# Kernel tuning notes

Hardware: AMD Instinct MI355X
Metric: run time of the kernel (lower is better)

## Reference

```python
import jax, jax.numpy as jnp
import numpy as np
import math

B, N, D_IN, D_OUT, H = 8, 1024, 512, 512, 8
DH = D_OUT // H  # 64
SCALE = math.sqrt(DH)

def setup_inputs() -> dict:
    key = jax.random.key(0)
    ks = jax.random.split(key, 10)
    s_in = 1.0 / math.sqrt(D_IN)
    s_out = 1.0 / math.sqrt(D_OUT)
    return {
        "x": jax.random.normal(ks[0], (B, N, D_IN), dtype=jnp.float32),
        "Wq": jax.random.uniform(ks[1], (D_IN, D_OUT), jnp.float32, -s_in, s_in),
        "bq": jnp.zeros((D_OUT,), jnp.float32),
        "Wk": jax.random.uniform(ks[2], (D_IN, D_OUT), jnp.float32, -s_in, s_in),
        "bk": jnp.zeros((D_OUT,), jnp.float32),
        "Wv": jax.random.uniform(ks[3], (D_IN, D_OUT), jnp.float32, -s_in, s_in),
        "bv": jnp.zeros((D_OUT,), jnp.float32),
        "Wo": jax.random.uniform(ks[4], (D_OUT, D_OUT), jnp.float32, -s_out, s_out),
        "bo": jnp.zeros((D_OUT,), jnp.float32),
        # external distance-based positional bias buffer (num_heads, N, N)
        "pos_bias": 0.01 * jax.random.normal(ks[5], (H, N, N), dtype=jnp.float32),
    }

def reference(x, Wq, bq, Wk, bk, Wv, bv, Wo, bo, pos_bias):
    Bx, Nx, _ = x.shape
    # QKV projections -> (B, H, N, DH)
    def split_heads(t):
        return t.reshape(Bx, Nx, H, DH).transpose(0, 2, 1, 3)
    q = split_heads(x @ Wq + bq)
    k = split_heads(x @ Wk + bk)
    v = split_heads(x @ Wv + bv)
    # scaled dot-product scores with additive positional bias
    scores = jnp.einsum('bhnd,bhmd->bhnm', q, k) / SCALE + pos_bias[None]
    attn = jax.nn.softmax(scores, axis=-1)  # dropout p=0 (eval)
    out = jnp.einsum('bhnm,bhmd->bhnd', attn, v)
    out = out.transpose(0, 2, 1, 3).reshape(Bx, Nx, D_OUT)  # concat heads
    return out @ Wo + bo
```

## Files before the change

### kernel.cpp

```cpp
#include <hip/hip_runtime.h>
#include <hip/hip_bf16.h>
#include <stdint.h>


typedef __attribute__((ext_vector_type(4))) float f32x4;
typedef __attribute__((ext_vector_type(8))) short s16x8;
typedef __attribute__((ext_vector_type(4))) unsigned short u16x4;
typedef __attribute__((ext_vector_type(8))) unsigned short u16x8;

union FragAB { s16x8 v; u16x4 h[2]; unsigned u[4]; };

#define LOG2E 1.44269504089f
#define QSCALE (0.125f * LOG2E)

__device__ __forceinline__ unsigned short f2b(float f) {
  unsigned u = __builtin_bit_cast(unsigned, f);
  u = (u + 0x7FFFu + ((u >> 16) & 1u)) >> 16;
  return (unsigned short)u;
}
__device__ __forceinline__ unsigned cvt_pk(float a, float b) {
  unsigned r;
  asm("v_cvt_pk_bf16_f32 %0, %1, %2" : "=v"(r) : "v"(a), "v"(b));
  return r;
}
__device__ __forceinline__ void gl_lds16(const unsigned short* g, unsigned short* l) {
  __builtin_amdgcn_global_load_lds(
      (const __attribute__((address_space(1))) unsigned int*)(g),
      (__attribute__((address_space(3))) unsigned int*)(l), 16, 0, 0);
}

__global__ __launch_bounds__(256) void prep_k(const float* __restrict__ x,
                                              unsigned short* __restrict__ xb,
                                              const float* __restrict__ W0,
                                              const float* __restrict__ W1,
                                              const float* __restrict__ W2,
                                              const float* __restrict__ W3,
                                              unsigned short* __restrict__ Wt) {
  __shared__ float ld[64][68];
  const int t = threadIdx.x;
  if (blockIdx.x < 4096) {
    int idx = blockIdx.x * 256 + t;
    f32x4 v = ((const f32x4*)x)[idx];
    u16x4 o;
#pragma unroll
    for (int j = 0; j < 4; j++) o[j] = f2b(v[j]);
    ((u16x4*)xb)[idx] = o;
    return;
  }
  const int bid2 = blockIdx.x - 4096;
  const int widx = bid2 >> 6;
  const int tile = bid2 & 63;
  const int trow = tile >> 3, tcol = tile & 7;
  const float* W = widx == 0 ? W0 : widx == 1 ? W1 : widx == 2 ? W2 : W3;
  const int r = t >> 2, cc = (t & 3) * 16;
  const float* src = W + (size_t)(trow * 64 + r) * 512 + tcol * 64 + cc;
#pragma unroll
  for (int u = 0; u < 4; u++)
    ((f32x4*)&ld[r][cc])[u] = ((const f32x4*)src)[u];
  __syncthreads();
  unsigned short* dst = Wt + ((size_t)widx << 18) + (size_t)(tcol * 64 + r) * 512 +
                        trow * 64 + cc;
#pragma unroll
  for (int u = 0; u < 4; u++) {
    u16x4 o;
#pragma unroll
    for (int e = 0; e < 4; e++) o[e] = f2b(ld[cc + u * 4 + e][r]);
    ((u16x4*)dst)[u] = o;
  }
}

__global__ __launch_bounds__(256, 2) void gemm_qkv_k(const unsigned short* __restrict__ A,
                                                     const unsigned short* __restrict__ Bt,
                                                     const float* __restrict__ bq,
                                                     const float* __restrict__ bk,
                                                     const float* __restrict__ bv,
                                                     unsigned short* __restrict__ outp) {
  __shared__ unsigned short SM[2][2][128][32];
  const int tid = threadIdx.x;
  const int lane = tid & 63;
  const int w = tid >> 6;
  const int wm = w >> 1, wn = w & 1;
  const int g = lane >> 4, c = lane & 15;
  const int bn0 = (blockIdx.x % 12) * 128;
  const int bm0 = (blockIdx.x / 12) * 128;

  f32x4 acc[4][4];
#pragma unroll
  for (int i = 0; i < 4; i++)
#pragma unroll
    for (int j = 0; j < 4; j++) acc[i][j] = f32x4{0.f, 0.f, 0.f, 0.f};

  auto stage = [&](int buf, int kt) {
#pragma unroll
    for (int j = 0; j < 2; j++) {
      const int qb = (j * 4 + w) * 64;
      const int chunk = qb + lane;
      const int row = chunk >> 2, slot = chunk & 3;
      gl_lds16(A + (size_t)(bm0 + row) * 512 + kt * 32 + slot * 8,
               &SM[buf][0][0][0] + qb * 8);
      gl_lds16(Bt + (size_t)(bn0 + row) * 512 + kt * 32 + slot * 8,
               &SM[buf][1][0][0] + qb * 8);
    }
  };

  stage(0, 0);
  asm volatile("s_waitcnt vmcnt(0)" ::: "memory");
  __syncthreads();

  for (int kt = 0; kt < 16; ++kt) {
    const int cb = kt & 1;
    if (kt < 15) stage(cb ^ 1, kt + 1);

    FragAB af[4], bf[4];
#pragma unroll
    for (int mi = 0; mi < 4; mi++) {
      const u16x4* p = (const u16x4*)&SM[cb][0][wm * 64 + mi * 16 + c][g * 8];
      af[mi].h[0] = p[0]; af[mi].h[1] = p[1];
    }
#pragma unroll
    for (int ni = 0; ni < 4; ni++) {
      const u16x4* p = (const u16x4*)&SM[cb][1][wn * 64 + ni * 16 + c][g * 8];
      bf[ni].h[0] = p[0]; bf[ni].h[1] = p[1];
    }
    __builtin_amdgcn_s_setprio(1);
#pragma unroll
    for (int mi = 0; mi < 4; mi++)
#pragma unroll
      for (int ni = 0; ni < 4; ni++)
        acc[mi][ni] = __builtin_amdgcn_mfma_f32_16x16x32_bf16(af[mi].v, bf[ni].v,
                                                              acc[mi][ni], 0, 0, 0);
    __builtin_amdgcn_s_setprio(0);

    if (kt < 15) {
      asm volatile("s_waitcnt vmcnt(0)" ::: "memory");
      __syncthreads();
    }
  }

  __syncthreads();

  const int qkv = (bn0 + wn * 64) >> 9;
  const float* bp = qkv == 0 ? bq : (qkv == 1 ? bk : bv);
  const float scale = qkv == 0 ? QSCALE : 1.0f;
  const int b = (bm0 + wm * 64) >> 10;
  const int nb = (bm0 + wm * 64) & 1023;

  if (qkv == 2) {
    unsigned short* T = &SM[0][0][0][0] + w * 2176;
    const int hh = ((bn0 + wn * 64) & 511) >> 6;
    unsigned short* dst = outp + ((size_t)2 << 22) + ((size_t)((b << 3) + hh) << 16) + nb;
#pragma unroll
    for (int r2 = 0; r2 < 2; r2++) {
#pragma unroll
      for (int ni2 = 0; ni2 < 2; ni2++) {
        const int ni = r2 * 2 + ni2;
        const int dloc = ni2 * 16 + c;
        const float bvv = bp[(bn0 + wn * 64 + ni * 16 + c) & 511];
#pragma unroll
        for (int mi = 0; mi < 4; mi++) {
          const int n = mi * 16 + g * 4;
          *(unsigned*)&T[dloc * 68 + n] =
              cvt_pk(acc[mi][ni][0] + bvv, acc[mi][ni][1] + bvv);
          *(unsigned*)&T[dloc * 68 + n + 2] =
              cvt_pk(acc[mi][ni][2] + bvv, acc[mi][ni][3] + bvv);
        }
      }
      asm volatile("s_waitcnt lgkmcnt(0)" ::: "memory");
#pragma unroll
      for (int r = 0; r < 8; r++) {
        const int dloc = r * 4 + g;
        const u16x4 v4 = *(const u16x4*)&T[dloc * 68 + c * 4];
        *(u16x4*)(dst + ((size_t)(r2 * 32 + dloc) << 10) + c * 4) = v4;
      }
      if (r2 == 0) asm volatile("s_waitcnt lgkmcnt(0)" ::: "memory");
    }
  } else {
#pragma unroll
    for (int mi = 0; mi < 4; mi++)
#pragma unroll
      for (int ni = 0; ni < 4; ni++) {
        const int c9 = (bn0 + wn * 64 + ni * 16 + c) & 511;
        const float bvv = bp[c9];
        const int hh = c9 >> 6, d = c9 & 63;
#pragma unroll
        for (int m = 0; m < 4; m++) {
          const int n = nb + mi * 16 + g * 4 + m;
          const float v = (acc[mi][ni][m] + bvv) * scale;
          outp[((size_t)qkv << 22) + ((size_t)((b << 3) + hh) << 16) +
               ((size_t)n << 6) + d] = f2b(v);
        }
      }
  }
}

__global__ __launch_bounds__(512, 2) void gemm_o_k(const unsigned short* __restrict__ A,
                                                   const unsigned short* __restrict__ Bt,
                                                   const float* __restrict__ bias,
                                                   float* __restrict__ outp) {
  __shared__ unsigned short SM[2][2][128][32];
  const int tid = threadIdx.x;
  const int lane = tid & 63;
  const int w = tid >> 6;
  const int wm = w >> 1, wn = w & 1;
  const int g = lane >> 4, c = lane & 15;
  const int bn0 = (blockIdx.x & 3) * 128;
  const int bm0 = (blockIdx.x >> 2) * 128;

  f32x4 acc[2][4];
#pragma unroll
  for (int i = 0; i < 2; i++)
#pragma unroll
    for (int j = 0; j < 4; j++) acc[i][j] = f32x4{0.f, 0.f, 0.f, 0.f};

  auto stage = [&](int buf, int kt) {
    const int qb = w * 64;
    const int chunk = qb + lane;
    const int row = chunk >> 2, slot = chunk & 3;
    gl_lds16(A + (size_t)(bm0 + row) * 512 + kt * 32 + slot * 8,
             &SM[buf][0][0][0] + qb * 8);
    gl_lds16(Bt + (size_t)(bn0 + row) * 512 + kt * 32 + slot * 8,
             &SM[buf][1][0][0] + qb * 8);
  };

  stage(0, 0);
  asm volatile("s_waitcnt vmcnt(0)" ::: "memory");
  __syncthreads();

  for (int kt = 0; kt < 16; ++kt) {
    const int cb = kt & 1;
    if (kt < 15) stage(cb ^ 1, kt + 1);

    FragAB af[2], bf[4];
#pragma unroll
    for (int mi = 0; mi < 2; mi++) {
      const u16x4* p = (const u16x4*)&SM[cb][0][wm * 32 + mi * 16 + c][g * 8];
      af[mi].h[0] = p[0]; af[mi].h[1] = p[1];
    }
#pragma unroll
    for (int ni = 0; ni < 4; ni++) {
      const u16x4* p = (const u16x4*)&SM[cb][1][wn * 64 + ni * 16 + c][g * 8];
      bf[ni].h[0] = p[0]; bf[ni].h[1] = p[1];
    }
    __builtin_amdgcn_s_setprio(1);
#pragma unroll
    for (int mi = 0; mi < 2; mi++)
#pragma unroll
      for (int ni = 0; ni < 4; ni++)
        acc[mi][ni] = __builtin_amdgcn_mfma_f32_16x16x32_bf16(af[mi].v, bf[ni].v,
                                                              acc[mi][ni], 0, 0, 0);
    __builtin_amdgcn_s_setprio(0);

    if (kt < 15) {
      asm volatile("s_waitcnt vmcnt(0)" ::: "memory");
      __syncthreads();
    }
  }

#pragma unroll
  for (int mi = 0; mi < 2; mi++) {
#pragma unroll
    for (int ni = 0; ni < 4; ni++) {
      const int col = bn0 + wn * 64 + ni * 16 + c;
      const float bv = bias[col];
#pragma unroll
      for (int m = 0; m < 4; m++) {
        const int row = bm0 + wm * 32 + mi * 16 + g * 4 + m;
        outp[(size_t)row * 512 + col] = acc[mi][ni][m] + bv;
      }
    }
  }
}

__global__ __launch_bounds__(256, 2) void attn_k(const unsigned short* __restrict__ Qb,
                                                 const unsigned short* __restrict__ Kb,
                                                 const unsigned short* __restrict__ Vt,
                                                 const float* __restrict__ pos_bias,
                                                 unsigned short* __restrict__ ao) {
  __shared__ unsigned short Klds[2][64][68];
  __shared__ unsigned short Vtlds[2][64][68];
  __shared__ unsigned short Plds[4][32][68];

  const int tid = threadIdx.x;
  const int lane = tid & 63;
  const int w = tid >> 6;
  const int g = lane >> 4, c = lane & 15;
  const int L = blockIdx.x;
  const int qt = L >> 6;
  const int bh = (L & 7) + 8 * ((L >> 3) & 7);
  const int h = bh & 7;
  const size_t bhq = (size_t)bh << 16;
  const int q0 = qt * 128 + w * 32;

  FragAB aq[2][2];
#pragma unroll
  for (int mi = 0; mi < 2; mi++)
#pragma unroll
    for (int kk = 0; kk < 2; kk++) {
      const u16x4* p = (const u16x4*)(Qb + bhq + ((size_t)(q0 + mi * 16 + c) << 6) +
                                      kk * 32 + g * 8);
      aq[mi][kk].h[0] = p[0]; aq[mi][kk].h[1] = p[1];
    }

  f32x4 acco[2][4];
#pragma unroll
  for (int mi = 0; mi < 2; mi++)
#pragma unroll
    for (int nd = 0; nd < 4; nd++) acco[mi][nd] = f32x4{0.f, 0.f, 0.f, 0.f};
  float lsum[2] = {0.f, 0.f};

  const int srow = tid >> 2;
  const int scol = (tid & 3) * 16;
  const unsigned short* pK = Kb + bhq + ((size_t)srow << 6) + scol;
  const unsigned short* pV = Vt + bhq + ((size_t)srow << 10) + scol;

  u16x8 kr0, kr1, vr0, vr1;
  auto stageLoad = [&](int k0n) {
    const u16x8* a = (const u16x8*)(pK + ((size_t)k0n << 6));
    kr0 = a[0]; kr1 = a[1];
    const u16x8* bb = (const u16x8*)(pV + k0n);
    vr0 = bb[0]; vr1 = bb[1];
  };
  auto stageWrite = [&](int b) {
    *(u16x8*)&Klds[b][srow][scol] = kr0;
    *(u16x8*)&Klds[b][srow][scol + 8] = kr1;
    *(u16x8*)&Vtlds[b][srow][scol] = vr0;
    *(u16x8*)&Vtlds[b][srow][scol + 8] = vr1;
  };

  const float* pbB = pos_bias + ((size_t)h << 20) + ((size_t)(q0 + c) << 10) + 4 * g;

  f32x4 pbA[2][4], pbC[2][4];
#pragma unroll
  for (int mi = 0; mi < 2; mi++)
#pragma unroll
    for (int ni = 0; ni < 4; ni++)
      pbA[mi][ni] = *(const f32x4*)(pbB + (mi << 14) + 16 * ni);

  stageLoad(0);
  stageWrite(0);
  __syncthreads();

  auto body = [&](int kt, f32x4 (&pbu)[2][4], f32x4 (&pbn)[2][4]) {
    const int buf = kt & 1;
    const int k0 = kt << 6;
    if (kt < 15) {
      stageLoad(k0 + 64);
#pragma unroll
      for (int mi = 0; mi < 2; mi++)
#pragma unroll
        for (int ni = 0; ni < 4; ni++)
          pbn[mi][ni] = *(const f32x4*)(pbB + (mi << 14) + k0 + 64 + 16 * ni);
    }

    FragAB bk[4][2];
#pragma unroll
    for (int ni = 0; ni < 4; ni++)
#pragma unroll
      for (int kk = 0; kk < 2; kk++) {
        const u16x4* p = (const u16x4*)&Klds[buf][ni * 16 + c][kk * 32 + g * 8];
        bk[ni][kk].h[0] = p[0]; bk[ni][kk].h[1] = p[1];
      }
    f32x4 sT[2][4];
    __builtin_amdgcn_s_setprio(1);
#pragma unroll
    for (int mi = 0; mi < 2; mi++)
#pragma unroll
      for (int ni = 0; ni < 4; ni++) {
        f32x4 s = f32x4{0.f, 0.f, 0.f, 0.f};
        s = __builtin_amdgcn_mfma_f32_16x16x32_bf16(bk[ni][0].v, aq[mi][0].v, s, 0, 0, 0);
        s = __builtin_amdgcn_mfma_f32_16x16x32_bf16(bk[ni][1].v, aq[mi][1].v, s, 0, 0, 0);
        sT[mi][ni] = s;
      }
    __builtin_amdgcn_s_setprio(0);

    FragAB vb2[4][2];
#pragma unroll
    for (int nd = 0; nd < 4; nd++)
#pragma unroll
      for (int kc = 0; kc < 2; kc++) {
        const u16x4* p = (const u16x4*)&Vtlds[buf][nd * 16 + c][kc * 32 + g * 8];
        vb2[nd][kc].h[0] = p[0]; vb2[nd][kc].h[1] = p[1];
      }

#pragma unroll
    for (int mi = 0; mi < 2; mi++)
#pragma unroll
      for (int ni = 0; ni < 4; ni++) {
        const float p0 = __builtin_amdgcn_exp2f(fmaf(pbu[mi][ni][0], LOG2E, sT[mi][ni][0]));
        const float p1 = __builtin_amdgcn_exp2f(fmaf(pbu[mi][ni][1], LOG2E, sT[mi][ni][1]));
        const float p2 = __builtin_amdgcn_exp2f(fmaf(pbu[mi][ni][2], LOG2E, sT[mi][ni][2]));
        const float p3 = __builtin_amdgcn_exp2f(fmaf(pbu[mi][ni][3], LOG2E, sT[mi][ni][3]));
        lsum[mi] += (p0 + p1) + (p2 + p3);
        uint2 two;
        two.x = cvt_pk(p0, p1);
        two.y = cvt_pk(p2, p3);
        *(uint2*)&Plds[w][mi * 16 + c][16 * ni + 4 * g] = two;
      }

    asm volatile("s_waitcnt lgkmcnt(0)" ::: "memory");

    FragAB paf[2][2];
#pragma unroll
    for (int mi = 0; mi < 2; mi++)
#pragma unroll
      for (int kc = 0; kc < 2; kc++) {
        const u16x4* p = (const u16x4*)&Plds[w][mi * 16 + c][kc * 32 + g * 8];
        paf[mi][kc].h[0] = p[0]; paf[mi][kc].h[1] = p[1];
      }
    __builtin_amdgcn_s_setprio(1);
#pragma unroll
    for (int mi = 0; mi < 2; mi++)
#pragma unroll
      for (int nd = 0; nd < 4; nd++) {
        acco[mi][nd] = __builtin_amdgcn_mfma_f32_16x16x32_bf16(paf[mi][0].v, vb2[nd][0].v,
                                                               acco[mi][nd], 0, 0, 0);
        acco[mi][nd] = __builtin_amdgcn_mfma_f32_16x16x32_bf16(paf[mi][1].v, vb2[nd][1].v,
                                                               acco[mi][nd], 0, 0, 0);
      }
    __builtin_amdgcn_s_setprio(0);

    if (kt < 15) {
      stageWrite(buf ^ 1);
      __syncthreads();
    }
  };

  for (int kt2 = 0; kt2 < 16; kt2 += 2) {
    body(kt2, pbA, pbC);
    body(kt2 + 1, pbC, pbA);
  }

  const int b = bh >> 3;
#pragma unroll
  for (int mi = 0; mi < 2; mi++) {
    float l = lsum[mi];
    l += __shfl_xor(l, 16);
    l += __shfl_xor(l, 32);
    const float inv_c = 1.f / l;
#pragma unroll
    for (int m = 0; m < 4; m++) {
      const float invm = __shfl(inv_c, g * 4 + m);
      const int n = q0 + mi * 16 + g * 4 + m;
#pragma unroll
      for (int nd = 0; nd < 4; nd++) {
        ao[((size_t)(b * 1024 + n) << 9) + h * 64 + nd * 16 + c] =
            f2b(acco[mi][nd][m] * invm);
      }
    }
  }
}

extern "C" void kernel_launch(void* const* d_in, const int* in_sizes, int n_in,
                              void* d_out, int out_size, void* d_ws, size_t ws_size,
                              hipStream_t stream) {
  (void)in_sizes; (void)n_in; (void)out_size; (void)ws_size;
  const float* x  = (const float*)d_in[0];
  const float* Wq = (const float*)d_in[1];
  const float* bq = (const float*)d_in[2];
  const float* Wk = (const float*)d_in[3];
  const float* bk = (const float*)d_in[4];
  const float* Wv = (const float*)d_in[5];
  const float* bv = (const float*)d_in[6];
  const float* Wo = (const float*)d_in[7];
  const float* bo = (const float*)d_in[8];
  const float* pbias = (const float*)d_in[9];

  char* p = (char*)d_ws;
  unsigned short* xb  = (unsigned short*)p; p += (size_t)8192 * 512 * 2;
  unsigned short* WT  = (unsigned short*)p; p += (size_t)4 * 512 * 512 * 2;
  unsigned short* Qb  = (unsigned short*)p; p += (size_t)3 * 64 * 1024 * 64 * 2;
  unsigned short* AO  = (unsigned short*)p;

  unsigned short* WoT = WT + (size_t)3 * 512 * 512;
  unsigned short* Kb  = Qb + (size_t)64 * 1024 * 64;
  unsigned short* Vb  = Kb + (size_t)64 * 1024 * 64;

  prep_k<<<4352, 256, 0, stream>>>(x, xb, Wq, Wk, Wv, Wo, WT);
  gemm_qkv_k<<<768, 256, 0, stream>>>(xb, WT, bq, bk, bv, Qb);
  attn_k<<<512, 256, 0, stream>>>(Qb, Kb, Vb, pbias, AO);
  gemm_o_k<<<256, 512, 0, stream>>>(AO, WoT, bo, (float*)d_out);
}
```

Baseline: 91.46 us.

## Run attention as single-wave blocks loading K/V fragments directly from global

The attention kernel shrinks from four-wave 256-thread blocks to one-wave 64-thread blocks, launching four times as many blocks. The double-buffered shared-memory staging of K and V, the block barriers and the software prefetch of pos_bias are removed. Each wave now reads its MFMA K/V fragments and bias straight from global memory inside the loop. This removes barrier and LDS-staging overhead, but K/V are no longer shared across waves, which multiplies cache traffic. It also exposes load latency because nothing is prefetched.

```diff
diff --git a/kernel.cpp b/kernel.cpp
--- a/kernel.cpp
+++ b/kernel.cpp
@@ -271,25 +271,21 @@
   }
 }
 
-__global__ __launch_bounds__(256, 2) void attn_k(const unsigned short* __restrict__ Qb,
-                                                 const unsigned short* __restrict__ Kb,
-                                                 const unsigned short* __restrict__ Vt,
-                                                 const float* __restrict__ pos_bias,
-                                                 unsigned short* __restrict__ ao) {
-  __shared__ unsigned short Klds[2][64][68];
-  __shared__ unsigned short Vtlds[2][64][68];
-  __shared__ unsigned short Plds[4][32][68];
-
-  const int tid = threadIdx.x;
-  const int lane = tid & 63;
-  const int w = tid >> 6;
+__global__ __launch_bounds__(64, 2) void attn_k(const unsigned short* __restrict__ Qb,
+                                                const unsigned short* __restrict__ Kb,
+                                                const unsigned short* __restrict__ Vt,
+                                                const float* __restrict__ pos_bias,
+                                                unsigned short* __restrict__ ao) {
+  __shared__ unsigned short Plds[32][68];
+
+  const int lane = threadIdx.x;
   const int g = lane >> 4, c = lane & 15;
   const int L = blockIdx.x;
   const int qt = L >> 6;
   const int bh = (L & 7) + 8 * ((L >> 3) & 7);
   const int h = bh & 7;
   const size_t bhq = (size_t)bh << 16;
-  const int q0 = qt * 128 + w * 32;
+  const int q0 = qt * 32;
 
   FragAB aq[2][2];
 #pragma unroll
@@ -308,58 +304,36 @@
     for (int nd = 0; nd < 4; nd++) acco[mi][nd] = f32x4{0.f, 0.f, 0.f, 0.f};
   float lsum[2] = {0.f, 0.f};
 
-  const int srow = tid >> 2;
-  const int scol = (tid & 3) * 16;
-  const unsigned short* pK = Kb + bhq + ((size_t)srow << 6) + scol;
-  const unsigned short* pV = Vt + bhq + ((size_t)srow << 10) + scol;
-
-  u16x8 kr0, kr1, vr0, vr1;
-  auto stageLoad = [&](int k0n) {
-    const u16x8* a = (const u16x8*)(pK + ((size_t)k0n << 6));
-    kr0 = a[0]; kr1 = a[1];
-    const u16x8* bb = (const u16x8*)(pV + k0n);
-    vr0 = bb[0]; vr1 = bb[1];
-  };
-  auto stageWrite = [&](int b) {
-    *(u16x8*)&Klds[b][srow][scol] = kr0;
-    *(u16x8*)&Klds[b][srow][scol + 8] = kr1;
-    *(u16x8*)&Vtlds[b][srow][scol] = vr0;
-    *(u16x8*)&Vtlds[b][srow][scol + 8] = vr1;
-  };
-
+  const unsigned short* pKb = Kb + bhq + ((size_t)c << 6) + g * 8;
+  const unsigned short* pVb = Vt + bhq + ((size_t)c << 10) + g * 8;
   const float* pbB = pos_bias + ((size_t)h << 20) + ((size_t)(q0 + c) << 10) + 4 * g;
 
-  f32x4 pbA[2][4], pbC[2][4];
-#pragma unroll
-  for (int mi = 0; mi < 2; mi++)
+  for (int kt = 0; kt < 16; ++kt) {
+    const int k0 = kt << 6;
+
+    FragAB bk[4][2];
 #pragma unroll
     for (int ni = 0; ni < 4; ni++)
-      pbA[mi][ni] = *(const f32x4*)(pbB + (mi << 14) + 16 * ni);
-
-  stageLoad(0);
-  stageWrite(0);
-  __syncthreads();
-
-  auto body = [&](int kt, f32x4 (&pbu)[2][4], f32x4 (&pbn)[2][4]) {
-    const int buf = kt & 1;
-    const int k0 = kt << 6;
-    if (kt < 15) {
-      stageLoad(k0 + 64);
-#pragma unroll
-      for (int mi = 0; mi < 2; mi++)
-#pragma unroll
-        for (int ni = 0; ni < 4; ni++)
-          pbn[mi][ni] = *(const f32x4*)(pbB + (mi << 14) + k0 + 64 + 16 * ni);
-    }
-
-    FragAB bk[4][2];
-#pragma unroll
-    for (int ni = 0; ni < 4; ni++)
 #pragma unroll
       for (int kk = 0; kk < 2; kk++) {
-        const u16x4* p = (const u16x4*)&Klds[buf][ni * 16 + c][kk * 32 + g * 8];
+        const u16x4* p = (const u16x4*)(pKb + (((size_t)(k0 + ni * 16)) << 6) + kk * 32);
         bk[ni][kk].h[0] = p[0]; bk[ni][kk].h[1] = p[1];
       }
+    FragAB vb2[4][2];
+#pragma unroll
+    for (int nd = 0; nd < 4; nd++)
+#pragma unroll
+      for (int kc = 0; kc < 2; kc++) {
+        const u16x4* p = (const u16x4*)(pVb + (((size_t)(nd * 16)) << 10) + k0 + kc * 32);
+        vb2[nd][kc].h[0] = p[0]; vb2[nd][kc].h[1] = p[1];
+      }
+    f32x4 pb[2][4];
+#pragma unroll
+    for (int mi = 0; mi < 2; mi++)
+#pragma unroll
+      for (int ni = 0; ni < 4; ni++)
+        pb[mi][ni] = *(const f32x4*)(pbB + (mi << 14) + k0 + 16 * ni);
+
     f32x4 sT[2][4];
     __builtin_amdgcn_s_setprio(1);
 #pragma unroll
@@ -373,28 +347,19 @@
       }
     __builtin_amdgcn_s_setprio(0);
 
-    FragAB vb2[4][2];
-#pragma unroll
-    for (int nd = 0; nd < 4; nd++)
-#pragma unroll
-      for (int kc = 0; kc < 2; kc++) {
-        const u16x4* p = (const u16x4*)&Vtlds[buf][nd * 16 + c][kc * 32 + g * 8];
-        vb2[nd][kc].h[0] = p[0]; vb2[nd][kc].h[1] = p[1];
-      }
-
 #pragma unroll
     for (int mi = 0; mi < 2; mi++)
 #pragma unroll
       for (int ni = 0; ni < 4; ni++) {
-        const float p0 = __builtin_amdgcn_exp2f(fmaf(pbu[mi][ni][0], LOG2E, sT[mi][ni][0]));
-        const float p1 = __builtin_amdgcn_exp2f(fmaf(pbu[mi][ni][1], LOG2E, sT[mi][ni][1]));
-        const float p2 = __builtin_amdgcn_exp2f(fmaf(pbu[mi][ni][2], LOG2E, sT[mi][ni][2]));
-        const float p3 = __builtin_amdgcn_exp2f(fmaf(pbu[mi][ni][3], LOG2E, sT[mi][ni][3]));
+        const float p0 = __builtin_amdgcn_exp2f(fmaf(pb[mi][ni][0], LOG2E, sT[mi][ni][0]));
+        const float p1 = __builtin_amdgcn_exp2f(fmaf(pb[mi][ni][1], LOG2E, sT[mi][ni][1]));
+        const float p2 = __builtin_amdgcn_exp2f(fmaf(pb[mi][ni][2], LOG2E, sT[mi][ni][2]));
+        const float p3 = __builtin_amdgcn_exp2f(fmaf(pb[mi][ni][3], LOG2E, sT[mi][ni][3]));
         lsum[mi] += (p0 + p1) + (p2 + p3);
         uint2 two;
         two.x = cvt_pk(p0, p1);
         two.y = cvt_pk(p2, p3);
-        *(uint2*)&Plds[w][mi * 16 + c][16 * ni + 4 * g] = two;
+        *(uint2*)&Plds[mi * 16 + c][16 * ni + 4 * g] = two;
       }
 
     asm volatile("s_waitcnt lgkmcnt(0)" ::: "memory");
@@ -404,7 +369,7 @@
     for (int mi = 0; mi < 2; mi++)
 #pragma unroll
       for (int kc = 0; kc < 2; kc++) {
-        const u16x4* p = (const u16x4*)&Plds[w][mi * 16 + c][kc * 32 + g * 8];
+        const u16x4* p = (const u16x4*)&Plds[mi * 16 + c][kc * 32 + g * 8];
         paf[mi][kc].h[0] = p[0]; paf[mi][kc].h[1] = p[1];
       }
     __builtin_amdgcn_s_setprio(1);
@@ -418,16 +383,6 @@
                                                                acco[mi][nd], 0, 0, 0);
       }
     __builtin_amdgcn_s_setprio(0);
-
-    if (kt < 15) {
-      stageWrite(buf ^ 1);
-      __syncthreads();
-    }
-  };
-
-  for (int kt2 = 0; kt2 < 16; kt2 += 2) {
-    body(kt2, pbA, pbC);
-    body(kt2 + 1, pbC, pbA);
   }
 
   const int b = bh >> 3;
@@ -477,6 +432,6 @@
 
   prep_k<<<4352, 256, 0, stream>>>(x, xb, Wq, Wk, Wv, Wo, WT);
   gemm_qkv_k<<<768, 256, 0, stream>>>(xb, WT, bq, bk, bv, Qb);
-  attn_k<<<512, 256, 0, stream>>>(Qb, Kb, Vb, pbias, AO);
+  attn_k<<<2048, 64, 0, stream>>>(Qb, Kb, Vb, pbias, AO);
   gemm_o_k<<<256, 512, 0, stream>>>(AO, WoT, bo, (float*)d_out);
 }
```

Result: slower. 132.4 us (+44.7%).

## Shrink attention tiles to 32 queries per 2-wave block for more parallelism

Applied to the files above, without the earlier changes.

The attention kernel now handles 32 query rows per block with 2 waves of 16 rows each, instead of 128 rows with 4 waves of 32 rows. The grid grows from 512 to 2048 blocks, and per-thread accumulator and fragment state shrinks. The goal is more blocks and waves in flight to hide latency and balance work across CUs. In exchange, each K/V tile is reused by 4x fewer queries, so K/V traffic through L2 rises. The pos_bias loads are also no longer prefetched one iteration ahead.

```diff
diff --git a/kernel.cpp b/kernel.cpp
--- a/kernel.cpp
+++ b/kernel.cpp
@@ -271,14 +271,14 @@
   }
 }
 
-__global__ __launch_bounds__(256, 2) void attn_k(const unsigned short* __restrict__ Qb,
+__global__ __launch_bounds__(128, 2) void attn_k(const unsigned short* __restrict__ Qb,
                                                  const unsigned short* __restrict__ Kb,
                                                  const unsigned short* __restrict__ Vt,
                                                  const float* __restrict__ pos_bias,
                                                  unsigned short* __restrict__ ao) {
   __shared__ unsigned short Klds[2][64][68];
   __shared__ unsigned short Vtlds[2][64][68];
-  __shared__ unsigned short Plds[4][32][68];
+  __shared__ unsigned short Plds[2][16][68];
 
   const int tid = threadIdx.x;
   const int lane = tid & 63;
@@ -289,68 +289,56 @@
   const int bh = (L & 7) + 8 * ((L >> 3) & 7);
   const int h = bh & 7;
   const size_t bhq = (size_t)bh << 16;
-  const int q0 = qt * 128 + w * 32;
-
-  FragAB aq[2][2];
-#pragma unroll
-  for (int mi = 0; mi < 2; mi++)
-#pragma unroll
-    for (int kk = 0; kk < 2; kk++) {
-      const u16x4* p = (const u16x4*)(Qb + bhq + ((size_t)(q0 + mi * 16 + c) << 6) +
-                                      kk * 32 + g * 8);
-      aq[mi][kk].h[0] = p[0]; aq[mi][kk].h[1] = p[1];
-    }
-
-  f32x4 acco[2][4];
-#pragma unroll
-  for (int mi = 0; mi < 2; mi++)
-#pragma unroll
-    for (int nd = 0; nd < 4; nd++) acco[mi][nd] = f32x4{0.f, 0.f, 0.f, 0.f};
-  float lsum[2] = {0.f, 0.f};
-
-  const int srow = tid >> 2;
-  const int scol = (tid & 3) * 16;
+  const int q0 = qt * 32 + w * 16;
+
+  FragAB aq[2];
+#pragma unroll
+  for (int kk = 0; kk < 2; kk++) {
+    const u16x4* p =
+        (const u16x4*)(Qb + bhq + ((size_t)(q0 + c) << 6) + kk * 32 + g * 8);
+    aq[kk].h[0] = p[0]; aq[kk].h[1] = p[1];
+  }
+
+  f32x4 acco[4];
+#pragma unroll
+  for (int nd = 0; nd < 4; nd++) acco[nd] = f32x4{0.f, 0.f, 0.f, 0.f};
+  float lsum = 0.f;
+
+  const int srow = tid >> 1;
+  const int scol = (tid & 1) * 32;
   const unsigned short* pK = Kb + bhq + ((size_t)srow << 6) + scol;
   const unsigned short* pV = Vt + bhq + ((size_t)srow << 10) + scol;
 
-  u16x8 kr0, kr1, vr0, vr1;
+  u16x8 kr[4], vr[4];
   auto stageLoad = [&](int k0n) {
     const u16x8* a = (const u16x8*)(pK + ((size_t)k0n << 6));
-    kr0 = a[0]; kr1 = a[1];
-    const u16x8* bb = (const u16x8*)(pV + k0n);
-    vr0 = bb[0]; vr1 = bb[1];
+    const u16x8* b = (const u16x8*)(pV + k0n);
+#pragma unroll
+    for (int j = 0; j < 4; j++) { kr[j] = a[j]; vr[j] = b[j]; }
   };
-  auto stageWrite = [&](int b) {
-    *(u16x8*)&Klds[b][srow][scol] = kr0;
-    *(u16x8*)&Klds[b][srow][scol + 8] = kr1;
-    *(u16x8*)&Vtlds[b][srow][scol] = vr0;
-    *(u16x8*)&Vtlds[b][srow][scol + 8] = vr1;
+  auto stageWrite = [&](int bf) {
+#pragma unroll
+    for (int j = 0; j < 4; j++) {
+      *(u16x8*)&Klds[bf][srow][scol + 8 * j] = kr[j];
+      *(u16x8*)&Vtlds[bf][srow][scol + 8 * j] = vr[j];
+    }
   };
 
   const float* pbB = pos_bias + ((size_t)h << 20) + ((size_t)(q0 + c) << 10) + 4 * g;
-
-  f32x4 pbA[2][4], pbC[2][4];
-#pragma unroll
-  for (int mi = 0; mi < 2; mi++)
-#pragma unroll
-    for (int ni = 0; ni < 4; ni++)
-      pbA[mi][ni] = *(const f32x4*)(pbB + (mi << 14) + 16 * ni);
 
   stageLoad(0);
   stageWrite(0);
   __syncthreads();
 
-  auto body = [&](int kt, f32x4 (&pbu)[2][4], f32x4 (&pbn)[2][4]) {
+  for (int kt = 0; kt < 16; ++kt) {
     const int buf = kt & 1;
     const int k0 = kt << 6;
-    if (kt < 15) {
-      stageLoad(k0 + 64);
-#pragma unroll
-      for (int mi = 0; mi < 2; mi++)
-#pragma unroll
-        for (int ni = 0; ni < 4; ni++)
-          pbn[mi][ni] = *(const f32x4*)(pbB + (mi << 14) + k0 + 64 + 16 * ni);
-    }
+    if (kt < 15) stageLoad(k0 + 64);
+
+    f32x4 pb[4];
+#pragma unroll
+    for (int ni = 0; ni < 4; ni++)
+      pb[ni] = *(const f32x4*)(pbB + k0 + 16 * ni);
 
     FragAB bk[4][2];
 #pragma unroll
@@ -360,17 +348,15 @@
         const u16x4* p = (const u16x4*)&Klds[buf][ni * 16 + c][kk * 32 + g * 8];
         bk[ni][kk].h[0] = p[0]; bk[ni][kk].h[1] = p[1];
       }
-    f32x4 sT[2][4];
+    f32x4 sT[4];
     __builtin_amdgcn_s_setprio(1);
 #pragma unroll
-    for (int mi = 0; mi < 2; mi++)
-#pragma unroll
-      for (int ni = 0; ni < 4; ni++) {
-        f32x4 s = f32x4{0.f, 0.f, 0.f, 0.f};
-        s = __builtin_amdgcn_mfma_f32_16x16x32_bf16(bk[ni][0].v, aq[mi][0].v, s, 0, 0, 0);
-        s = __builtin_amdgcn_mfma_f32_16x16x32_bf16(bk[ni][1].v, aq[mi][1].v, s, 0, 0, 0);
-        sT[mi][ni] = s;
-      }
+    for (int ni = 0; ni < 4; ni++) {
+      f32x4 s = f32x4{0.f, 0.f, 0.f, 0.f};
+      s = __builtin_amdgcn_mfma_f32_16x16x32_bf16(bk[ni][0].v, aq[0].v, s, 0, 0, 0);
+      s = __builtin_amdgcn_mfma_f32_16x16x32_bf16(bk[ni][1].v, aq[1].v, s, 0, 0, 0);
+      sT[ni] = s;
+    }
     __builtin_amdgcn_s_setprio(0);
 
     FragAB vb2[4][2];
@@ -383,69 +369,55 @@
       }
 
 #pragma unroll
-    for (int mi = 0; mi < 2; mi++)
-#pragma unroll
-      for (int ni = 0; ni < 4; ni++) {
-        const float p0 = __builtin_amdgcn_exp2f(fmaf(pbu[mi][ni][0], LOG2E, sT[mi][ni][0]));
-        const float p1 = __builtin_amdgcn_exp2f(fmaf(pbu[mi][ni][1], LOG2E, sT[mi][ni][1]));
-        const float p2 = __builtin_amdgcn_exp2f(fmaf(pbu[mi][ni][2], LOG2E, sT[mi][ni][2]));
-        const float p3 = __builtin_amdgcn_exp2f(fmaf(pbu[mi][ni][3], LOG2E, sT[mi][ni][3]));
-        lsum[mi] += (p0 + p1) + (p2 + p3);
-        uint2 two;
-        two.x = cvt_pk(p0, p1);
-        two.y = cvt_pk(p2, p3);
-        *(uint2*)&Plds[w][mi * 16 + c][16 * ni + 4 * g] = two;
-      }
+    for (int ni = 0; ni < 4; ni++) {
+      const float p0 = __builtin_amdgcn_exp2f(fmaf(pb[ni][0], LOG2E, sT[ni][0]));
+      const float p1 = __builtin_amdgcn_exp2f(fmaf(pb[ni][1], LOG2E, sT[ni][1]));
+      const float p2 = __builtin_amdgcn_exp2f(fmaf(pb[ni][2], LOG2E, sT[ni][2]));
+      const float p3 = __builtin_amdgcn_exp2f(fmaf(pb[ni][3], LOG2E, sT[ni][3]));
+      lsum += (p0 + p1) + (p2 + p3);
+      uint2 two;
+      two.x = cvt_pk(p0, p1);
+      two.y = cvt_pk(p2, p3);
+      *(uint2*)&Plds[w][c][16 * ni + 4 * g] = two;
+    }
 
     asm volatile("s_waitcnt lgkmcnt(0)" ::: "memory");
 
-    FragAB paf[2][2];
-#pragma unroll
-    for (int mi = 0; mi < 2; mi++)
-#pragma unroll
-      for (int kc = 0; kc < 2; kc++) {
-        const u16x4* p = (const u16x4*)&Plds[w][mi * 16 + c][kc * 32 + g * 8];
-        paf[mi][kc].h[0] = p[0]; paf[mi][kc].h[1] = p[1];
-      }
+    FragAB paf[2];
+#pragma unroll
+    for (int kc = 0; kc < 2; kc++) {
+      const u16x4* p = (const u16x4*)&Plds[w][c][kc * 32 + g * 8];
+      paf[kc].h[0] = p[0]; paf[kc].h[1] = p[1];
+    }
     __builtin_amdgcn_s_setprio(1);
 #pragma unroll
-    for (int mi = 0; mi < 2; mi++)
-#pragma unroll
-      for (int nd = 0; nd < 4; nd++) {
-        acco[mi][nd] = __builtin_amdgcn_mfma_f32_16x16x32_bf16(paf[mi][0].v, vb2[nd][0].v,
-                                                               acco[mi][nd], 0, 0, 0);
-        acco[mi][nd] = __builtin_amdgcn_mfma_f32_16x16x32_bf16(paf[mi][1].v, vb2[nd][1].v,
-                                                               acco[mi][nd], 0, 0, 0);
-      }
+    for (int nd = 0; nd < 4; nd++) {
+      acco[nd] = __builtin_amdgcn_mfma_f32_16x16x32_bf16(paf[0].v, vb2[nd][0].v,
+                                                         acco[nd], 0, 0, 0);
+      acco[nd] = __builtin_amdgcn_mfma_f32_16x16x32_bf16(paf[1].v, vb2[nd][1].v,
+                                                         acco[nd], 0, 0, 0);
+    }
     __builtin_amdgcn_s_setprio(0);
 
     if (kt < 15) {
       stageWrite(buf ^ 1);
       __syncthreads();
     }
-  };
-
-  for (int kt2 = 0; kt2 < 16; kt2 += 2) {
-    body(kt2, pbA, pbC);
-    body(kt2 + 1, pbC, pbA);
   }
 
   const int b = bh >> 3;
-#pragma unroll
-  for (int mi = 0; mi < 2; mi++) {
-    float l = lsum[mi];
-    l += __shfl_xor(l, 16);
-    l += __shfl_xor(l, 32);
-    const float inv_c = 1.f / l;
-#pragma unroll
-    for (int m = 0; m < 4; m++) {
-      const float invm = __shfl(inv_c, g * 4 + m);
-      const int n = q0 + mi * 16 + g * 4 + m;
-#pragma unroll
-      for (int nd = 0; nd < 4; nd++) {
-        ao[((size_t)(b * 1024 + n) << 9) + h * 64 + nd * 16 + c] =
-            f2b(acco[mi][nd][m] * invm);
-      }
+  float l = lsum;
+  l += __shfl_xor(l, 16);
+  l += __shfl_xor(l, 32);
+  const float inv_c = 1.f / l;
+#pragma unroll
+  for (int m = 0; m < 4; m++) {
+    const float invm = __shfl(inv_c, g * 4 + m);
+    const int n = q0 + g * 4 + m;
+#pragma unroll
+    for (int nd = 0; nd < 4; nd++) {
+      ao[((size_t)(b * 1024 + n) << 9) + h * 64 + nd * 16 + c] =
+          f2b(acco[nd][m] * invm);
     }
   }
 }
@@ -477,6 +449,6 @@
 
   prep_k<<<4352, 256, 0, stream>>>(x, xb, Wq, Wk, Wv, Wo, WT);
   gemm_qkv_k<<<768, 256, 0, stream>>>(xb, WT, bq, bk, bv, Qb);
-  attn_k<<<512, 256, 0, stream>>>(Qb, Kb, Vb, pbias, AO);
+  attn_k<<<2048, 128, 0, stream>>>(Qb, Kb, Vb, pbias, AO);
   gemm_o_k<<<256, 512, 0, stream>>>(AO, WoT, bo, (float*)d_out);
 }
```

Result: slower. 113.7 us (+24.3%).
